# Kernel tuning notes

Measured on AMD Instinct MI355X. Metric: run time of the kernel, lower is better.

## Reference

```python
import jax, jax.numpy as jnp
import numpy as np

B, S, E = 4, 2048, 2048
H = 16
DH = 2048 // H  # head dim = 128


def setup_inputs() -> dict:
    key = jax.random.key(0)
    k0, k1, k2, k3 = jax.random.split(key, 4)
    scale = 1.0 / np.sqrt(E)
    embedded = jax.random.normal(k0, (B, S, E), dtype=jnp.float32)
    # stacked per-head projection weights, bias-free Linear: y = x @ W^T -> store as [H, E, DH]
    Wq = jax.random.normal(k1, (H, E, DH), dtype=jnp.float32) * scale
    Wk = jax.random.normal(k2, (H, E, DH), dtype=jnp.float32) * scale
    Wv = jax.random.normal(k3, (H, E, DH), dtype=jnp.float32) * scale
    return {"embedded": embedded, "Wq": Wq, "Wk": Wk, "Wv": Wv}


def reference(embedded, Wq, Wk, Wv):
    # batched over heads instead of the original python loop (same math)
    q = jnp.einsum("bse,hed->bhsd", embedded, Wq)
    k = jnp.einsum("bse,hed->bhsd", embedded, Wk)
    v = jnp.einsum("bse,hed->bhsd", embedded, Wv)
    scores = jnp.einsum("bhsd,bhtd->bhst", q, k) / jnp.sqrt(jnp.float32(DH))
    causal = jnp.tril(jnp.ones((S, S), dtype=bool))  # [S, S]
    scores = jnp.where(causal, scores, -jnp.inf)
    probs = jax.nn.softmax(scores, axis=-1)
    out = jnp.einsum("bhst,bhtd->bhsd", probs, v)
    cated = out.transpose(0, 2, 1, 3).reshape(B, S, H * DH)  # concat heads on dim=2
    return jnp.round(cated, 4)
```

## Files before the change

kernel.cpp:

```cpp
#include <hip/hip_runtime.h>

typedef float   f32x4 __attribute__((ext_vector_type(4)));
typedef _Float16 half8 __attribute__((ext_vector_type(8)));
typedef _Float16 half4 __attribute__((ext_vector_type(4)));

#define B_  4
#define S_  2048
#define E_  2048
#define H_  16
#define DH_ 128

__device__ __forceinline__ void gld16(const void* g, void* l) {
  __builtin_amdgcn_global_load_lds((const void __attribute__((address_space(1)))*)g,
                                   (void __attribute__((address_space(3)))*)l, 16, 0, 0);
}

__global__ __launch_bounds__(256) void k_prep(const float* __restrict__ X, _Float16* __restrict__ Xh,
    const float* __restrict__ Wq, const float* __restrict__ Wk, const float* __restrict__ Wv,
    _Float16* __restrict__ Wqt, _Float16* __restrict__ Wkt, _Float16* __restrict__ Wvt) {
  const int bid = blockIdx.x;
  const int tid = threadIdx.x;
  if (bid < 8192) {
    size_t i = ((size_t)bid * 256 + tid) * 8;
    float4 a = *(const float4*)(X + i);
    float4 b = *(const float4*)(X + i + 4);
    half8 h;
    h[0]=(_Float16)a.x; h[1]=(_Float16)a.y; h[2]=(_Float16)a.z; h[3]=(_Float16)a.w;
    h[4]=(_Float16)b.x; h[5]=(_Float16)b.y; h[6]=(_Float16)b.z; h[7]=(_Float16)b.w;
    *(half8*)(Xh + i) = h;
  } else {
    __shared__ float t[32][33];
    const int wi = bid - 8192;
    const int e0 = (wi & 63) * 32;
    const int d0 = ((wi >> 6) & 3) * 32;
    const int pz = wi >> 8;
    const int p = pz >> 4, h = pz & 15;
    const float* W  = (p==0) ? Wq  : (p==1) ? Wk  : Wv;
    _Float16*    Wt = (p==0) ? Wqt : (p==1) ? Wkt : Wvt;
    const int tx = tid & 31, ty = tid >> 5;
    for (int i=0;i<4;i++)
      t[ty+8*i][tx] = W[((size_t)h*E_ + (e0+ty+8*i))*DH_ + d0+tx];
    __syncthreads();
    for (int i=0;i<4;i++)
      Wt[((size_t)h*DH_ + (d0+ty+8*i))*E_ + e0+tx] = (_Float16)t[tx][ty+8*i];
  }
}

#define NT 32

__global__ __launch_bounds__(512, 2) void k_gemm(const _Float16* __restrict__ X,
    const _Float16* __restrict__ Wq, const _Float16* __restrict__ Wk, const _Float16* __restrict__ Wv,
    _Float16* __restrict__ Qo, _Float16* __restrict__ Ko, _Float16* __restrict__ Vt)
{
  __shared__ __align__(16) _Float16 pool[65536];

  const int z = blockIdx.z;
  const _Float16* Wp = (z==0) ? Wq : (z==1) ? Wk : Wv;

  const int fi  = blockIdx.x + (blockIdx.y << 5);
  const int xcd = fi & 7, kk_ = fi >> 3;
  const int lbx = ((xcd >> 1) << 3) | (kk_ & 7);
  const int lby = ((xcd & 1) << 2) | (kk_ >> 3);
  const int m0 = lbx << 8, n0 = lby << 8;

  const int tid = threadIdx.x;
  const int wid = tid >> 6, lane = tid & 63, quad = lane >> 4, lcol = lane & 15;
  const int wm = wid >> 2, wn = wid & 3;

  int soff[2]; int slds[2];
  #pragma unroll
  for (int r=0;r<2;r++){
    int chunk = wid*128 + r*64 + lane;
    int row = chunk >> 3, cl = chunk & 7, cg = cl ^ (row & 7);
    soff[r] = row*E_ + cg*8;
    slds[r] = (wid*128 + r*64) * 16;
  }

  const _Float16* Ag = X  + (size_t)m0 * E_;
  const _Float16* Bg = Wp + (size_t)n0 * E_;

  auto stageA = [&](int mh, int tt, int buf){
    const _Float16* s = Ag + mh*(128*E_) + tt*64;
    char* l = (char*)pool + (buf*4096 + mh*1024)*16;
    #pragma unroll
    for (int r=0;r<2;r++) gld16(s + soff[r], l + slds[r]);
  };
  auto stageB = [&](int nh, int tt, int buf){
    const _Float16* s = Bg + nh*(128*E_) + tt*64;
    char* l = (char*)pool + (buf*4096 + (2+nh)*1024)*16;
    #pragma unroll
    for (int r=0;r<2;r++) gld16(s + soff[r], l + slds[r]);
  };

  half8 a[2][4], b[2][2];
  f32x4 acc[2][2][4][2] = {};

  auto rdA = [&](int mh, int buf){
    const _Float16* base = pool + (buf*4096 + mh*1024)*8;
    #pragma unroll
    for (int kk=0;kk<2;kk++)
      #pragma unroll
      for (int mi=0;mi<4;mi++){
        int R = wm*64 + mi*16 + lcol;
        int c = (kk*4 + quad) ^ (R & 7);
        a[kk][mi] = *(const half8*)(base + R*64 + c*8);
      }
  };
  auto rdB = [&](int nh, int buf){
    const _Float16* base = pool + (buf*4096 + (2+nh)*1024)*8;
    #pragma unroll
    for (int kk=0;kk<2;kk++)
      #pragma unroll
      for (int ni=0;ni<2;ni++){
        int R = wn*32 + ni*16 + lcol;
        int c = (kk*4 + quad) ^ (R & 7);
        b[kk][ni] = *(const half8*)(base + R*64 + c*8);
      }
  };
  auto mm = [&](f32x4 (&ac)[4][2]){
    #pragma unroll
    for (int kk=0;kk<2;kk++)
      #pragma unroll
      for (int mi=0;mi<4;mi++)
        #pragma unroll
        for (int ni=0;ni<2;ni++)
          ac[mi][ni] = __builtin_amdgcn_mfma_f32_16x16x32_f16(a[kk][mi], b[kk][ni], ac[mi][ni], 0, 0, 0);
  };

  stageA(0,0,0); stageB(0,0,0); stageA(1,0,0); stageB(1,0,0);
  stageA(0,1,1); stageB(1,1,1); stageA(1,1,1);
  asm volatile("s_waitcnt vmcnt(6)" ::: "memory");
  __builtin_amdgcn_s_barrier();

#define MFMA_OPEN() do{ __builtin_amdgcn_s_barrier(); \
    asm volatile("s_waitcnt lgkmcnt(0)" ::: "memory"); \
    __builtin_amdgcn_sched_barrier(0); \
    __builtin_amdgcn_s_setprio(1); }while(0)
#define MFMA_CLOSE() do{ __builtin_amdgcn_s_setprio(0); \
    __builtin_amdgcn_s_barrier(); }while(0)

#define TILE(T, BUF) do{ \
    rdA(0, BUF); rdB(0, BUF); \
    if ((T)+1 < NT) stageB(0, (T)+1, (BUF)^1); \
    MFMA_OPEN(); mm(acc[0][0]); MFMA_CLOSE(); \
    rdB(1, BUF); \
    if ((T)+2 < NT) stageA(0, (T)+2, BUF); \
    MFMA_OPEN(); mm(acc[0][1]); MFMA_CLOSE(); \
    rdA(1, BUF); \
    if ((T)+2 < NT) stageB(1, (T)+2, BUF); \
    MFMA_OPEN(); mm(acc[1][1]); MFMA_CLOSE(); \
    rdB(0, BUF); \
    if ((T)+2 < NT) stageA(1, (T)+2, BUF); \
    __builtin_amdgcn_s_barrier(); \
    asm volatile("s_waitcnt lgkmcnt(0)" ::: "memory"); \
    __builtin_amdgcn_sched_barrier(0); \
    __builtin_amdgcn_s_setprio(1); \
    mm(acc[1][0]); \
    __builtin_amdgcn_s_setprio(0); \
    if ((T) < NT-2)       { asm volatile("s_waitcnt vmcnt(6)" ::: "memory"); } \
    else if ((T) == NT-2) { asm volatile("s_waitcnt vmcnt(0)" ::: "memory"); } \
    __builtin_amdgcn_s_barrier(); \
  }while(0)

  for (int t = 0; t < NT; t += 2){
    TILE(t,   0);
    TILE(t+1, 1);
  }
#undef TILE
#undef MFMA_OPEN
#undef MFMA_CLOSE

  const int bb = m0 >> 11;
  const int s0 = m0 & 2047;
  const int h0 = n0 >> 7;
  if (z < 2){
    _Float16* O = z ? Ko : Qo;
    #pragma unroll
    for (int mh=0; mh<2; mh++)
      #pragma unroll
      for (int nh=0; nh<2; nh++)
        #pragma unroll
        for (int mi=0; mi<4; mi++)
          #pragma unroll
          for (int ni=0; ni<2; ni++){
            const int srow = s0 + mh*128 + wm*64 + mi*16 + quad*4;
            const int d = wn*32 + ni*16 + lcol;
            _Float16* p = O + (((size_t)bb*H_ + (h0+nh))*S_ + srow)*DH_ + d;
            const f32x4 v = acc[mh][nh][mi][ni];
            p[0]=(_Float16)v[0]; p[DH_]=(_Float16)v[1]; p[2*DH_]=(_Float16)v[2]; p[3*DH_]=(_Float16)v[3];
          }
  } else {
    #pragma unroll
    for (int mh=0; mh<2; mh++)
      #pragma unroll
      for (int nh=0; nh<2; nh++)
        #pragma unroll
        for (int mi=0; mi<4; mi++)
          #pragma unroll
          for (int ni=0; ni<2; ni++){
            const int scol = s0 + mh*128 + wm*64 + mi*16 + quad*4;
            const int d = wn*32 + ni*16 + lcol;
            const f32x4 u = acc[mh][nh][mi][ni];
            half4 v;
            v[0]=(_Float16)u[0]; v[1]=(_Float16)u[1]; v[2]=(_Float16)u[2]; v[3]=(_Float16)u[3];
            *(half4*)(Vt + (((size_t)bb*H_ + (h0+nh))*DH_ + d)*S_ + scol) = v;
          }
  }
}

__global__ __launch_bounds__(512, 2) void k_attn(const _Float16* __restrict__ Q,
    const _Float16* __restrict__ K, const _Float16* __restrict__ Vt, float* __restrict__ out)
{
  __shared__ __align__(16) _Float16 Ks[2][8192], Vs[2][8192];

  const int b = blockIdx.z, h = blockIdx.y;
  const int qsel = (b < 2) ? (7 - (int)blockIdx.x) : (int)blockIdx.x;
  const int q0 = qsel * 256;
  const int tid = threadIdx.x, wid = tid >> 6, lane = tid & 63, quad = lane >> 4, lcol = lane & 15;
  const size_t bh = (size_t)b*H_ + h;
  const _Float16* Qg = Q  + (bh*S_ + q0)*DH_;
  const _Float16* Kg = K  + bh*S_*DH_;
  const _Float16* Vg = Vt + bh*DH_*S_;

  int krow[2], kcg[2], vdr[2], vcg[2];
  for (int r=0;r<2;r++){
    int chunk = wid*128 + r*64 + lane;
    krow[r] = chunk >> 4;
    kcg[r]  = (chunk & 15) ^ (krow[r] & 15);
    vdr[r]  = chunk >> 3;
    vcg[r]  = (chunk & 7) ^ (vdr[r] & 7);
  }

  half8 qf[2][4];
  for (int g=0; g<2; g++)
    for (int kk=0; kk<4; kk++)
      qf[g][kk] = *(const half8*)(Qg + (size_t)(wid*32 + g*16 + lcol)*DH_ + kk*32 + quad*8);

  for (int r=0;r<2;r++){
    gld16(Kg + (size_t)krow[r]*DH_ + kcg[r]*8, (char*)Ks[0] + wid*2048 + r*1024 + lane*16);
    gld16(Vg + (size_t)vdr[r]*S_ + 0 + vcg[r]*8, (char*)Vs[0] + wid*2048 + r*1024 + lane*16);
  }

  f32x4 oaccT[2][8] = {};
  f32x4 lacc[2] = {};
  const half4 ones = {(_Float16)1.f,(_Float16)1.f,(_Float16)1.f,(_Float16)1.f};
  const float c1 = 0.12751879526654326f;
  const float c2 = -11.541560327111707f;
  const int rbase = q0 + wid*32;
  const int nt = (q0 >> 6) + 4;

  for (int t = 0; t < nt; t++) {
    const int buf = t & 1;
    const _Float16* ksb = Ks[buf];
    const _Float16* vsb = Vs[buf];
    const int j0 = t << 6;
    const bool live0 = (j0 <= rbase + 15);
    const bool live1 = (j0 <= rbase + 31);
    __syncthreads();

    f32x4 sa[2][4] = {};
    if (live0){
      __builtin_amdgcn_s_setprio(1);
      for (int kk=0; kk<4; kk++){
        int cl = (kk*4 + quad) ^ lcol;
        for (int jb=0; jb<4; jb++){
          half8 kf = *(const half8*)(ksb + (size_t)(jb*16 + lcol)*DH_ + cl*8);
          sa[0][jb] = __builtin_amdgcn_mfma_f32_16x16x32_f16(kf, qf[0][kk], sa[0][jb], 0, 0, 0);
          sa[1][jb] = __builtin_amdgcn_mfma_f32_16x16x32_f16(kf, qf[1][kk], sa[1][jb], 0, 0, 0);
        }
      }
      __builtin_amdgcn_s_setprio(0);
    } else if (live1){
      __builtin_amdgcn_s_setprio(1);
      for (int kk=0; kk<4; kk++){
        int cl = (kk*4 + quad) ^ lcol;
        for (int jb=0; jb<4; jb++){
          half8 kf = *(const half8*)(ksb + (size_t)(jb*16 + lcol)*DH_ + cl*8);
          sa[1][jb] = __builtin_amdgcn_mfma_f32_16x16x32_f16(kf, qf[1][kk], sa[1][jb], 0, 0, 0);
        }
      }
      __builtin_amdgcn_s_setprio(0);
    }

    if (t+1 < nt){
      const int j1 = (t+1) << 6;
      for (int r=0;r<2;r++){
        gld16(Kg + (size_t)(j1+krow[r])*DH_ + kcg[r]*8, (char*)Ks[buf^1] + wid*2048 + r*1024 + lane*16);
        gld16(Vg + (size_t)vdr[r]*S_ + j1 + vcg[r]*8,   (char*)Vs[buf^1] + wid*2048 + r*1024 + lane*16);
      }
    }

    if (live1){
      half4 pb[2][4];
      auto sm = [&](f32x4 (&s4)[4], half4 (&p4)[4], int rb){
        if (j0 + 63 > rb){
          for (int jb=0; jb<4; jb++)
            for (int rg=0; rg<4; rg++){
              int j = jb*16 + quad*4 + rg;
              float p = (j0 + j > rb + lcol) ? 0.f
                      : __builtin_amdgcn_exp2f(fmaf(s4[jb][rg], c1, c2));
              p4[jb][rg] = (_Float16)p;
            }
        } else {
          for (int jb=0; jb<4; jb++)
            for (int rg=0; rg<4; rg++)
              p4[jb][rg] = (_Float16)__builtin_amdgcn_exp2f(fmaf(s4[jb][rg], c1, c2));
        }
      };

      if (live0){
        sm(sa[0], pb[0], rbase);
        sm(sa[1], pb[1], rbase + 16);
        __builtin_amdgcn_s_setprio(1);
        for (int jb=0; jb<4; jb++){
          lacc[0] = __builtin_amdgcn_mfma_f32_16x16x16f16(ones, pb[0][jb], lacc[0], 0, 0, 0);
          lacc[1] = __builtin_amdgcn_mfma_f32_16x16x16f16(ones, pb[1][jb], lacc[1], 0, 0, 0);
        }
        for (int dblk=0; dblk<8; dblk++){
          const _Float16* vrow = vsb + (size_t)(dblk*16 + lcol)*64;
          for (int jb=0; jb<4; jb++){
            int cl = (2*jb + (quad>>1)) ^ (lcol & 7);
            half4 va = *(const half4*)(vrow + cl*8 + (quad&1)*4);
            oaccT[0][dblk] = __builtin_amdgcn_mfma_f32_16x16x16f16(va, pb[0][jb], oaccT[0][dblk], 0, 0, 0);
            oaccT[1][dblk] = __builtin_amdgcn_mfma_f32_16x16x16f16(va, pb[1][jb], oaccT[1][dblk], 0, 0, 0);
          }
        }
        __builtin_amdgcn_s_setprio(0);
      } else {
        sm(sa[1], pb[1], rbase + 16);
        __builtin_amdgcn_s_setprio(1);
        for (int jb=0; jb<4; jb++)
          lacc[1] = __builtin_amdgcn_mfma_f32_16x16x16f16(ones, pb[1][jb], lacc[1], 0, 0, 0);
        for (int dblk=0; dblk<8; dblk++){
          const _Float16* vrow = vsb + (size_t)(dblk*16 + lcol)*64;
          for (int jb=0; jb<4; jb++){
            int cl = (2*jb + (quad>>1)) ^ (lcol & 7);
            half4 va = *(const half4*)(vrow + cl*8 + (quad&1)*4);
            oaccT[1][dblk] = __builtin_amdgcn_mfma_f32_16x16x16f16(va, pb[1][jb], oaccT[1][dblk], 0, 0, 0);
          }
        }
        __builtin_amdgcn_s_setprio(0);
      }
    }
  }

  for (int g=0; g<2; g++){
    const float rinv = 1.f / lacc[g][0];
    const int s = q0 + wid*32 + g*16 + lcol;
    float* op = out + ((size_t)b*S_ + s)*(H_*DH_) + h*DH_ + quad*4;
    for (int dblk=0; dblk<8; dblk++){
      float4 v;
      v.x = oaccT[g][dblk][0]*rinv; v.y = oaccT[g][dblk][1]*rinv;
      v.z = oaccT[g][dblk][2]*rinv; v.w = oaccT[g][dblk][3]*rinv;
      *(float4*)(op + dblk*16) = v;
    }
  }
}

extern "C" void kernel_launch(void* const* d_in, const int* in_sizes, int n_in,
                              void* d_out, int out_size, void* d_ws, size_t ws_size,
                              hipStream_t stream) {
  const float* X  = (const float*)d_in[0];
  const float* Wq = (const float*)d_in[1];
  const float* Wk = (const float*)d_in[2];
  const float* Wv = (const float*)d_in[3];
  float* out = (float*)d_out;

  _Float16* Xh  = (_Float16*)d_ws;
  _Float16* Wqt = Xh  + (size_t)B_*S_*E_;
  _Float16* Wkt = Wqt + (size_t)H_*E_*DH_;
  _Float16* Wvt = Wkt + (size_t)H_*E_*DH_;
  _Float16* Qh  = Wvt + (size_t)H_*E_*DH_;
  _Float16* Kh  = Qh  + (size_t)B_*H_*S_*DH_;
  _Float16* Vth = Kh  + (size_t)B_*H_*S_*DH_;

  k_prep<<<8192 + 12288, 256, 0, stream>>>(X, Xh, Wq, Wk, Wv, Wqt, Wkt, Wvt);
  k_gemm<<<dim3(32, 8, 3), 512, 0, stream>>>(Xh, Wqt, Wkt, Wvt, Qh, Kh, Vth);
  k_attn<<<dim3(S_/256, H_, B_), 512, 0, stream>>>(Qh, Kh, Vth, out);
}
```

Baseline: 447.7 us.

## Halve GEMM K-tile to 32 and software-pipeline LDS fragment reads across MFMA phases

```diff
diff --git a/kernel.cpp b/kernel.cpp
--- a/kernel.cpp
+++ b/kernel.cpp
@@ -46,13 +46,13 @@
   }
 }
 
-#define NT 32
+#define NT 64
 
 __global__ __launch_bounds__(512, 2) void k_gemm(const _Float16* __restrict__ X,
     const _Float16* __restrict__ Wq, const _Float16* __restrict__ Wk, const _Float16* __restrict__ Wv,
     _Float16* __restrict__ Qo, _Float16* __restrict__ Ko, _Float16* __restrict__ Vt)
 {
-  __shared__ __align__(16) _Float16 pool[65536];
+  __shared__ __align__(16) _Float16 pool[32768];
 
   const int z = blockIdx.z;
   const _Float16* Wp = (z==0) ? Wq : (z==1) ? Wk : Wv;
@@ -67,108 +67,125 @@
   const int wid = tid >> 6, lane = tid & 63, quad = lane >> 4, lcol = lane & 15;
   const int wm = wid >> 2, wn = wid & 3;
 
-  int soff[2]; int slds[2];
-  #pragma unroll
-  for (int r=0;r<2;r++){
-    int chunk = wid*128 + r*64 + lane;
-    int row = chunk >> 3, cl = chunk & 7, cg = cl ^ (row & 7);
-    soff[r] = row*E_ + cg*8;
-    slds[r] = (wid*128 + r*64) * 16;
-  }
+  const int srow = tid >> 2;
+  const int scg  = (tid & 3) ^ (srow & 3);
+  const int soff = srow * E_ + scg * 8;
+  const int sldsb = wid * 1024;
 
   const _Float16* Ag = X  + (size_t)m0 * E_;
   const _Float16* Bg = Wp + (size_t)n0 * E_;
 
-  auto stageA = [&](int mh, int tt, int buf){
-    const _Float16* s = Ag + mh*(128*E_) + tt*64;
-    char* l = (char*)pool + (buf*4096 + mh*1024)*16;
-    #pragma unroll
-    for (int r=0;r<2;r++) gld16(s + soff[r], l + slds[r]);
-  };
-  auto stageB = [&](int nh, int tt, int buf){
-    const _Float16* s = Bg + nh*(128*E_) + tt*64;
-    char* l = (char*)pool + (buf*4096 + (2+nh)*1024)*16;
-    #pragma unroll
-    for (int r=0;r<2;r++) gld16(s + soff[r], l + slds[r]);
-  };
-
-  half8 a[2][4], b[2][2];
+  auto stA = [&](int mh, int tt, int buf){
+    gld16(Ag + (size_t)mh*(128*E_) + tt*32 + soff,
+          (char*)pool + buf*32768 + mh*8192 + sldsb);
+  };
+  auto stB = [&](int nh, int tt, int buf){
+    gld16(Bg + (size_t)nh*(128*E_) + tt*32 + soff,
+          (char*)pool + buf*32768 + (2+nh)*8192 + sldsb);
+  };
+
+  half8 fa0[4], fa1[4], fb0[2], fb1[2];
   f32x4 acc[2][2][4][2] = {};
 
-  auto rdA = [&](int mh, int buf){
-    const _Float16* base = pool + (buf*4096 + mh*1024)*8;
-    #pragma unroll
-    for (int kk=0;kk<2;kk++)
+  const int rc = quad ^ (lcol & 3);
+
+  auto rdA = [&](half8* d, int mh, int buf){
+    const _Float16* base = pool + buf*16384 + mh*4096;
+    #pragma unroll
+    for (int mi=0; mi<4; mi++){
+      int R = wm*64 + mi*16 + lcol;
+      d[mi] = *(const half8*)(base + R*32 + rc*8);
+    }
+  };
+  auto rdB = [&](half8* d, int nh, int buf){
+    const _Float16* base = pool + buf*16384 + (2+nh)*4096;
+    #pragma unroll
+    for (int ni=0; ni<2; ni++){
+      int R = wn*32 + ni*16 + lcol;
+      d[ni] = *(const half8*)(base + R*32 + rc*8);
+    }
+  };
+  auto mm = [&](f32x4 (&ac)[4][2], const half8* av, const half8* bv){
+    #pragma unroll
+    for (int mi=0; mi<4; mi++)
       #pragma unroll
-      for (int mi=0;mi<4;mi++){
-        int R = wm*64 + mi*16 + lcol;
-        int c = (kk*4 + quad) ^ (R & 7);
-        a[kk][mi] = *(const half8*)(base + R*64 + c*8);
-      }
-  };
-  auto rdB = [&](int nh, int buf){
-    const _Float16* base = pool + (buf*4096 + (2+nh)*1024)*8;
-    #pragma unroll
-    for (int kk=0;kk<2;kk++)
-      #pragma unroll
-      for (int ni=0;ni<2;ni++){
-        int R = wn*32 + ni*16 + lcol;
-        int c = (kk*4 + quad) ^ (R & 7);
-        b[kk][ni] = *(const half8*)(base + R*64 + c*8);
-      }
-  };
-  auto mm = [&](f32x4 (&ac)[4][2]){
-    #pragma unroll
-    for (int kk=0;kk<2;kk++)
-      #pragma unroll
-      for (int mi=0;mi<4;mi++)
-        #pragma unroll
-        for (int ni=0;ni<2;ni++)
-          ac[mi][ni] = __builtin_amdgcn_mfma_f32_16x16x32_f16(a[kk][mi], b[kk][ni], ac[mi][ni], 0, 0, 0);
-  };
-
-  stageA(0,0,0); stageB(0,0,0); stageA(1,0,0); stageB(1,0,0);
-  stageA(0,1,1); stageB(1,1,1); stageA(1,1,1);
-  asm volatile("s_waitcnt vmcnt(6)" ::: "memory");
+      for (int ni=0; ni<2; ni++)
+        ac[mi][ni] = __builtin_amdgcn_mfma_f32_16x16x32_f16(av[mi], bv[ni], ac[mi][ni], 0, 0, 0);
+  };
+
+#define WOPEN() do{ __builtin_amdgcn_s_barrier(); \
+    asm volatile("s_waitcnt lgkmcnt(0)" ::: "memory"); \
+    __builtin_amdgcn_sched_barrier(0); }while(0)
+#define SB() __builtin_amdgcn_sched_barrier(0)
+#define PRIO1() __builtin_amdgcn_s_setprio(1)
+#define PRIO0() __builtin_amdgcn_s_setprio(0)
+
+#define TILE_EVEN(T, G1, G2, VM) do{ \
+     \
+    WOPEN(); rdB(fb1, 1, 0); SB(); \
+    PRIO1(); mm(acc[0][0], fa0, fb0); PRIO0(); \
+    if (G1) stB(0, (T)+1, 1); \
+     \
+    WOPEN(); rdA(fa1, 1, 0); SB(); \
+    PRIO1(); mm(acc[0][1], fa0, fb1); PRIO0(); \
+    if (G2) stA(0, (T)+2, 0); \
+     \
+    WOPEN(); \
+    PRIO1(); mm(acc[1][1], fa1, fb1); PRIO0(); \
+    if (G2) stB(1, (T)+2, 0); \
+     \
+    if (VM == 2)      { asm volatile("s_waitcnt vmcnt(2)" ::: "memory"); } \
+    else if (VM == 0) { asm volatile("s_waitcnt vmcnt(0)" ::: "memory"); } \
+    WOPEN(); \
+    if (G1) { rdA(fa0, 0, 1); rdB(fb1, 1, 1); } SB(); \
+    PRIO1(); mm(acc[1][0], fa1, fb0); PRIO0(); \
+    if (G2) stA(1, (T)+2, 0); \
+  }while(0)
+
+#define TILE_ODD(T, G1, G2, VM) do{ \
+     \
+    WOPEN(); rdB(fb0, 0, 1); SB(); \
+    PRIO1(); mm(acc[0][1], fa0, fb1); PRIO0(); \
+    if (G1) stB(0, (T)+1, 0); \
+     \
+    WOPEN(); rdA(fa1, 1, 1); SB(); \
+    PRIO1(); mm(acc[0][0], fa0, fb0); PRIO0(); \
+    if (G2) stA(0, (T)+2, 1); \
+     \
+    WOPEN(); \
+    PRIO1(); mm(acc[1][0], fa1, fb0); PRIO0(); \
+    if (G2) stB(1, (T)+2, 1); \
+     \
+    if (VM == 2)      { asm volatile("s_waitcnt vmcnt(2)" ::: "memory"); } \
+    else if (VM == 0) { asm volatile("s_waitcnt vmcnt(0)" ::: "memory"); } \
+    WOPEN(); \
+    if (G1) { rdA(fa0, 0, 0); rdB(fb0, 0, 0); } SB(); \
+    PRIO1(); mm(acc[1][1], fa1, fb1); PRIO0(); \
+    if (G2) stA(1, (T)+2, 1); \
+  }while(0)
+
+  stA(0,0,0); stB(0,0,0); stA(1,0,0); stB(1,0,0);
+  stA(0,1,1); stB(1,1,1);
+  asm volatile("s_waitcnt vmcnt(2)" ::: "memory");
+  stA(1,1,1);
   __builtin_amdgcn_s_barrier();
-
-#define MFMA_OPEN() do{ __builtin_amdgcn_s_barrier(); \
-    asm volatile("s_waitcnt lgkmcnt(0)" ::: "memory"); \
-    __builtin_amdgcn_sched_barrier(0); \
-    __builtin_amdgcn_s_setprio(1); }while(0)
-#define MFMA_CLOSE() do{ __builtin_amdgcn_s_setprio(0); \
-    __builtin_amdgcn_s_barrier(); }while(0)
-
-#define TILE(T, BUF) do{ \
-    rdA(0, BUF); rdB(0, BUF); \
-    if ((T)+1 < NT) stageB(0, (T)+1, (BUF)^1); \
-    MFMA_OPEN(); mm(acc[0][0]); MFMA_CLOSE(); \
-    rdB(1, BUF); \
-    if ((T)+2 < NT) stageA(0, (T)+2, BUF); \
-    MFMA_OPEN(); mm(acc[0][1]); MFMA_CLOSE(); \
-    rdA(1, BUF); \
-    if ((T)+2 < NT) stageB(1, (T)+2, BUF); \
-    MFMA_OPEN(); mm(acc[1][1]); MFMA_CLOSE(); \
-    rdB(0, BUF); \
-    if ((T)+2 < NT) stageA(1, (T)+2, BUF); \
-    __builtin_amdgcn_s_barrier(); \
-    asm volatile("s_waitcnt lgkmcnt(0)" ::: "memory"); \
-    __builtin_amdgcn_sched_barrier(0); \
-    __builtin_amdgcn_s_setprio(1); \
-    mm(acc[1][0]); \
-    __builtin_amdgcn_s_setprio(0); \
-    if ((T) < NT-2)       { asm volatile("s_waitcnt vmcnt(6)" ::: "memory"); } \
-    else if ((T) == NT-2) { asm volatile("s_waitcnt vmcnt(0)" ::: "memory"); } \
-    __builtin_amdgcn_s_barrier(); \
-  }while(0)
-
-  for (int t = 0; t < NT; t += 2){
-    TILE(t,   0);
-    TILE(t+1, 1);
-  }
-#undef TILE
-#undef MFMA_OPEN
-#undef MFMA_CLOSE
+  rdA(fa0, 0, 0); rdB(fb0, 0, 0);
+
+  for (int t = 0; t < NT-4; t += 2){
+    TILE_EVEN(t,   1, 1, 2);
+    TILE_ODD (t+1, 1, 1, 2);
+  }
+  TILE_EVEN(NT-4, 1, 1, 2);
+  TILE_ODD (NT-3, 1, 1, 2);
+  TILE_EVEN(NT-2, 1, 0, 0);
+  TILE_ODD (NT-1, 0, 0, -1);
+
+#undef TILE_EVEN
+#undef TILE_ODD
+#undef WOPEN
+#undef SB
+#undef PRIO1
+#undef PRIO0
 
   const int bb = m0 >> 11;
   const int s0 = m0 & 2047;
@@ -183,9 +200,9 @@
         for (int mi=0; mi<4; mi++)
           #pragma unroll
           for (int ni=0; ni<2; ni++){
-            const int srow = s0 + mh*128 + wm*64 + mi*16 + quad*4;
+            const int srw = s0 + mh*128 + wm*64 + mi*16 + quad*4;
             const int d = wn*32 + ni*16 + lcol;
-            _Float16* p = O + (((size_t)bb*H_ + (h0+nh))*S_ + srow)*DH_ + d;
+            _Float16* p = O + (((size_t)bb*H_ + (h0+nh))*S_ + srw)*DH_ + d;
             const f32x4 v = acc[mh][nh][mi][ni];
             p[0]=(_Float16)v[0]; p[DH_]=(_Float16)v[1]; p[2*DH_]=(_Float16)v[2]; p[3*DH_]=(_Float16)v[3];
           }
```

Result: faster. 431.1 us (-3.7%).
